# Kernel optimization log

Hardware: AMD Instinct MI355X
Metric: run time of the kernel (lower is better)

The kernel has to match this reference:

```python
import jax, jax.numpy as jnp
import numpy as np

N_NODES = 100000
N_EDGES = 1600000
K_IND = 16          # num_indicator_weight (distance bins)
K_MLP = 16          # num_mlp_weight
DIM_HIDDEN = 64     # dim_mlp_hidden
DIST_MAX = 1.0      # distance_max
K = K_IND + K_MLP   # node feature dim / Dense output dim


def setup_inputs() -> dict:
    key = jax.random.key(0)
    ks = jax.random.split(key, 10)
    nodes = jax.random.normal(ks[0], (N_NODES, K), dtype=jnp.float32)
    distance = jax.random.uniform(ks[1], (N_EDGES,), dtype=jnp.float32) * DIST_MAX
    receivers = jnp.sort(jax.random.randint(ks[2], (N_EDGES,), 0, N_NODES, dtype=jnp.int32))
    senders = jax.random.randint(ks[3], (N_EDGES,), 0, N_NODES, dtype=jnp.int32)
    edges_padding = jnp.ones((N_EDGES,), dtype=jnp.float32)
    # MLPWeights params (Dense(1->H), Dense(H->K_MLP))
    w1 = jax.random.normal(ks[4], (1, DIM_HIDDEN), dtype=jnp.float32) / np.sqrt(1.0)
    b1 = jnp.zeros((DIM_HIDDEN,), dtype=jnp.float32)
    w2 = jax.random.normal(ks[5], (DIM_HIDDEN, K_MLP), dtype=jnp.float32) / np.sqrt(DIM_HIDDEN)
    b2 = jnp.zeros((K_MLP,), dtype=jnp.float32)
    # PowerDifference params (a=0.5, b=2)
    a = jnp.array([0.5], dtype=jnp.float32)
    b = jnp.array([2.0], dtype=jnp.float32)
    # gamma_self (no bias), gamma_gathered (with bias), both Dense(K->K)
    wg_self = jax.random.normal(ks[6], (K, K), dtype=jnp.float32) / np.sqrt(K)
    wg_gath = jax.random.normal(ks[7], (K, K), dtype=jnp.float32) / np.sqrt(K)
    bg_gath = jnp.zeros((K,), dtype=jnp.float32)
    return {"nodes": nodes, "distance": distance, "edges_padding": edges_padding,
            "receivers": receivers, "senders": senders,
            "w1": w1, "b1": b1, "w2": w2, "b2": b2,
            "a": a, "b": b, "wg_self": wg_self, "wg_gath": wg_gath, "bg_gath": bg_gath}


def _normalize_edges(edges, seg_ids, num_segments):
    sums = jax.ops.segment_sum(edges, seg_ids, num_segments=num_segments, indices_are_sorted=True)
    return edges / (sums[seg_ids] + 1e-5)


def _softmax_edges(edges, seg_ids, num_segments):
    maxs = jax.ops.segment_max(edges, seg_ids, num_segments=num_segments, indices_are_sorted=True)
    e = jnp.exp(edges - maxs[seg_ids])
    sums = jax.ops.segment_sum(e, seg_ids, num_segments=num_segments, indices_are_sorted=True)
    return e / sums[seg_ids]


def reference(nodes, distance, edges_padding, receivers, senders,
              w1, b1, w2, b2, a, b, wg_self, wg_gath, bg_gath):
    n = nodes.shape[0]
    d = distance[:, None]                                   # [E,1]
    # IndicatorWeights: bin membership via heaviside of product
    bins = jnp.linspace(0.0, DIST_MAX, K_IND + 1, dtype=nodes.dtype)
    indicator = jnp.heaviside((bins[None, :-1] - d) * (d - bins[None, 1:]), 0.0)  # [E,K_IND]
    indicator_w = _normalize_edges(indicator, receivers, n)
    # MLPWeights: Dense -> relu -> Dense, then segment softmax
    mlp = jax.nn.relu(d @ w1 + b1) @ w2 + b2                # [E,K_MLP]
    mlp_w = _softmax_edges(mlp, receivers, n)
    weights = jnp.concatenate([indicator_w, mlp_w], axis=1) * edges_padding[:, None]  # [E,K]
    # PowerDifference on gathered node pairs
    a_c = jnp.clip(a, 0.0, 1.0)
    b_c = jnp.abs(b)
    edge_pds = jnp.power(jnp.abs(a_c * nodes[receivers] - (1.0 - a_c) * nodes[senders]), b_c)  # [E,K]
    gathered = jax.ops.segment_sum(weights * edge_pds, receivers, num_segments=n, indices_are_sorted=True)  # [N,K]
    out = jax.nn.relu(nodes @ wg_self + (gathered @ wg_gath + bg_gath))
    return out
```

## Files before the change

### kernel.cpp

```cpp
#include <hip/hip_runtime.h>
#include <math.h>

#define K_TOT 32
#define K_IND 16
#define K_MLP 16
#define DHID  64


__global__ void prep_kernel(const int* __restrict__ recv, int E, int N,
                            const float* __restrict__ w1,
                            const float* __restrict__ b1,
                            const float* __restrict__ w2,
                            float* __restrict__ wsP,
                            float* __restrict__ wsN,
                            int* __restrict__ wsflag,
                            int* __restrict__ rp) {
    if (blockIdx.x == 0 && threadIdx.x < 64) {
        int t = threadIdx.x;
        if (t < K_MLP) {
            float P = 0.f, Nn = 0.f;
            for (int j = 0; j < DHID; ++j) {
                float w = w1[j];
                float v = w2[j * K_MLP + t];
                P  += fmaxf(w, 0.f) * v;
                Nn += fminf(w, 0.f) * v;
            }
            wsP[t] = P; wsN[t] = Nn;
        }
        bool nz = (b1[t] != 0.f);
        unsigned long long mask = __ballot(nz);
        if (t == 0) *wsflag = (mask == 0ull) ? 1 : 0;
    }
    int tid = blockIdx.x * blockDim.x + threadIdx.x;
    if (tid <= N) {
        int lo = 0, hi = E;
        while (lo < hi) {
            int mid = (lo + hi) >> 1;
            if (recv[mid] < tid) lo = mid + 1; else hi = mid;
        }
        rp[tid] = lo;
    }
}

__global__ __launch_bounds__(256) void graph_kernel(
        const float* __restrict__ nodes,
        const float* __restrict__ dist,
        const float* __restrict__ padv,
        const int*   __restrict__ send,
        const float* __restrict__ w1,
        const float* __restrict__ b1,
        const float* __restrict__ w2,
        const float* __restrict__ b2,
        const float* __restrict__ a_p,
        const float* __restrict__ b_p,
        const float* __restrict__ wg_self,
        const float* __restrict__ wg_gath,
        const float* __restrict__ bg,
        const float* __restrict__ wsP,
        const float* __restrict__ wsN,
        const int*   __restrict__ wsflag,
        const int*   __restrict__ rp,
        float* __restrict__ out,
        int N) {
    int wave = blockIdx.x * (blockDim.x >> 6) + (threadIdx.x >> 6);
    if (wave >= N) return;
    int n    = wave;
    int lane = threadIdx.x & 63;
    int eg   = lane >> 4;
    int cc   = lane & 15;

    float a_c = fminf(fmaxf(a_p[0], 0.f), 1.f);
    float am  = 1.f - a_c;
    float bc  = fabsf(b_p[0]);
    bool  fastf = (*wsflag != 0) && (bc == 2.0f);

    float Pk = wsP[cc];
    float Nk = wsN[cc];

    const float* nrow = nodes + n * K_TOT;
    float nr0 = nrow[cc];
    float nr1 = nrow[cc + 16];
    float anr0 = a_c * nr0;
    float anr1 = a_c * nr1;

    int e0 = rp[n], eEnd = rp[n + 1];
    int len = eEnd - e0;

    float lo = (float)cc * 0.0625f;
    float hi = lo + 0.0625f;

    float cnt = 0.f, si = 0.f;
    float l = 0.f, acc = 0.f;
    float g_ind, g_mlp;

    int egb = eg << 2;

    if (__builtin_amdgcn_readfirstlane((int)fastf)) {
        float dm = 0.f;
        for (int base = 0; base < len; base += 64) {
            int idx = base + lane;
            int cmax = len - 1;
            idx = idx < cmax ? idx : cmax;
            dm = fmaxf(dm, fabsf(dist[e0 + idx]));
        }
#pragma unroll
        for (int off = 32; off; off >>= 1) dm = fmaxf(dm, __shfl_xor(dm, off));
        float negM = -fmaxf(fabsf(Pk), fabsf(Nk)) * dm;

        for (int base = 0; base < len; base += 64) {
            int rem = len - base;
            int ci = base + lane;
            int cmax = len - 1;
            ci = ci < cmax ? ci : cmax;
            int e = e0 + ci;
            float dl = dist[e];
            int   sl = send[e];
            float pl = padv[e];
            int nG = (rem + 3) >> 2;
            nG = nG < 16 ? nG : 16;
            int byteIdx = egb;
            for (int g2 = 0; g2 < nG; ++g2, byteIdx += 16) {
                float d  = __int_as_float(__builtin_amdgcn_ds_bpermute(byteIdx, __float_as_int(dl)));
                int   s  = __builtin_amdgcn_ds_bpermute(byteIdx, sl);
                float pe = __int_as_float(__builtin_amdgcn_ds_bpermute(byteIdx, __float_as_int(pl)));
                bool valid = (base + (g2 << 2) + eg) < len;

                const float* nsrow = nodes + (s * K_TOT + cc);
                float ns0 = nsrow[0];
                float ns1 = nsrow[16];

                float t0 = fmaf(-am, ns0, anr0);
                float t1 = fmaf(-am, ns1, anr1);
                float pd0 = t0 * t0;
                float pd1 = t1 * t1;

                bool inb = valid && (d > lo) && (d < hi);
                cnt += inb ? 1.f : 0.f;
                si  += inb ? pe * pd0 : 0.f;

                float q = (d > 0.f) ? Pk : Nk;
                float p = __expf(fmaf(d, q, negM));
                p = valid ? p : 0.f;
                l += p;
                acc = fmaf(p, pe * pd1, acc);
            }
        }

#pragma unroll
        for (int off = 16; off <= 32; off <<= 1) {
            cnt += __shfl_xor(cnt, off);
            si  += __shfl_xor(si,  off);
            l   += __shfl_xor(l,   off);
            acc += __shfl_xor(acc, off);
        }
        g_ind = si / (cnt + 1e-5f);
        g_mlp = (l > 0.f) ? (acc / l) : 0.f;
    } else {
        float m_on = -INFINITY;
        for (int i = eg; i < len; i += 4) {
            int e = e0 + i;
            float d  = dist[e];
            int   s  = send[e];
            float pe = padv[e];
            const float* nsrow = nodes + (s * K_TOT + cc);
            float ns0 = nsrow[0];
            float ns1 = nsrow[16];
            float t0 = fabsf(fmaf(-am, ns0, anr0));
            float t1 = fabsf(fmaf(-am, ns1, anr1));
            float pd0 = powf(t0, bc);
            float pd1 = powf(t1, bc);

            bool inb = (d > lo) && (d < hi);
            cnt += inb ? 1.f : 0.f;
            si  += inb ? pe * pd0 : 0.f;

            float mlp = 0.f;
            for (int j = 0; j < DHID; ++j) {
                float h = fmaxf(fmaf(d, w1[j], b1[j]), 0.f);
                mlp = fmaf(h, w2[j * K_MLP + cc], mlp);
            }
            float mn = fmaxf(m_on, mlp);
            float al = (m_on == -INFINITY) ? 0.f : __expf(m_on - mn);
            float p  = __expf(mlp - mn);
            l   = fmaf(l, al, p);
            acc = fmaf(acc, al, p * pe * pd1);
            m_on = mn;
        }
#pragma unroll
        for (int off = 16; off <= 32; off <<= 1) {
            cnt += __shfl_xor(cnt, off);
            si  += __shfl_xor(si,  off);
            float m2 = __shfl_xor(m_on, off), l2 = __shfl_xor(l, off), a2 = __shfl_xor(acc, off);
            float mn = fmaxf(m_on, m2);
            float f1 = (m_on == -INFINITY) ? 0.f : __expf(m_on - mn);
            float f2 = (m2   == -INFINITY) ? 0.f : __expf(m2 - mn);
            l   = l * f1 + l2 * f2;
            acc = acc * f1 + a2 * f2;
            m_on = mn;
        }
        g_ind = si / (cnt + 1e-5f);
        g_mlp = (l > 0.f) ? (acc / l) : 0.f;
    }

    int h  = lane >> 5;
    int oc = lane & 31;
    float pre_g = ((lane >> 4) & 1) ? g_mlp : g_ind;
    float pre_n = ((lane >> 4) & 1) ? nr1 : nr0;

    float o = 0.f;
    int jbase = h * 16;
#pragma unroll
    for (int jj = 0; jj < 16; ++jj) {
        int j = jbase + jj;
        float gj = __shfl(pre_g, j);
        float nj = __shfl(pre_n, j);
        o = fmaf(nj, wg_self[j * K_TOT + oc], o);
        o = fmaf(gj, wg_gath[j * K_TOT + oc], o);
    }
    o += __shfl_xor(o, 32);
    if (h == 0) {
        out[n * K_TOT + oc] = fmaxf(o + bg[oc], 0.f);
    }
}

extern "C" void kernel_launch(void* const* d_in, const int* in_sizes, int n_in,
                              void* d_out, int out_size, void* d_ws, size_t ws_size,
                              hipStream_t stream) {
    const float* nodes   = (const float*)d_in[0];
    const float* dist    = (const float*)d_in[1];
    const float* padv    = (const float*)d_in[2];
    const int*   recv    = (const int*)d_in[3];
    const int*   send    = (const int*)d_in[4];
    const float* w1      = (const float*)d_in[5];
    const float* b1      = (const float*)d_in[6];
    const float* w2      = (const float*)d_in[7];
    const float* b2      = (const float*)d_in[8];
    const float* a_p     = (const float*)d_in[9];
    const float* b_p     = (const float*)d_in[10];
    const float* wg_self = (const float*)d_in[11];
    const float* wg_gath = (const float*)d_in[12];
    const float* bg      = (const float*)d_in[13];
    float* out = (float*)d_out;

    int N = in_sizes[0] / K_TOT;
    int E = in_sizes[1];

    float* wsf    = (float*)d_ws;
    float* wsP    = wsf;
    float* wsN    = wsf + 16;
    int*   wsflag = (int*)d_ws + 32;
    int*   rp     = (int*)d_ws + 64;

    prep_kernel<<<(N + 1 + 255) / 256, 256, 0, stream>>>(recv, E, N, w1, b1, w2,
                                                         wsP, wsN, wsflag, rp);
    graph_kernel<<<(N + 3) / 4, 256, 0, stream>>>(
        nodes, dist, padv, send, w1, b1, w2, b2, a_p, b_p,
        wg_self, wg_gath, bg, wsP, wsN, wsflag, rp, out, N);
}
```

Baseline: 179.0 us.

## Process four nodes per wavefront, one 16-lane quarter per node

Measured after the change: 214.0 us. +19.6%, slower.

```diff
diff --git a/kernel.cpp b/kernel.cpp
--- a/kernel.cpp
+++ b/kernel.cpp
@@ -42,7 +42,7 @@
     }
 }
 
-__global__ __launch_bounds__(256) void graph_kernel(
+__global__ __launch_bounds__(256) void graph4_kernel(
         const float* __restrict__ nodes,
         const float* __restrict__ dist,
         const float* __restrict__ padv,
@@ -50,7 +50,6 @@
         const float* __restrict__ w1,
         const float* __restrict__ b1,
         const float* __restrict__ w2,
-        const float* __restrict__ b2,
         const float* __restrict__ a_p,
         const float* __restrict__ b_p,
         const float* __restrict__ wg_self,
@@ -62,29 +61,28 @@
         const int*   __restrict__ rp,
         float* __restrict__ out,
         int N) {
-    int wave = blockIdx.x * (blockDim.x >> 6) + (threadIdx.x >> 6);
-    if (wave >= N) return;
-    int n    = wave;
+    int wave  = blockIdx.x * 4 + (threadIdx.x >> 6);
+    int nbase = wave * 4;
+    if (nbase >= N) return;
     int lane = threadIdx.x & 63;
-    int eg   = lane >> 4;
+    int q    = lane >> 4;
     int cc   = lane & 15;
 
     float a_c = fminf(fmaxf(a_p[0], 0.f), 1.f);
     float am  = 1.f - a_c;
     float bc  = fabsf(b_p[0]);
-    bool  fastf = (*wsflag != 0) && (bc == 2.0f);
-
-    float Pk = wsP[cc];
-    float Nk = wsN[cc];
-
-    const float* nrow = nodes + n * K_TOT;
-    float nr0 = nrow[cc];
-    float nr1 = nrow[cc + 16];
-    float anr0 = a_c * nr0;
-    float anr1 = a_c * nr1;
-
-    int e0 = rp[n], eEnd = rp[n + 1];
-    int len = eEnd - e0;
+    float Pk  = wsP[cc];
+    float Nk  = wsN[cc];
+
+    int n  = nbase + q;
+    int nl = (n < N) ? n : N - 1;
+    int e0 = rp[nl], e1 = rp[nl + 1];
+    int len = (n < N) ? (e1 - e0) : 0;
+    int eb  = (len > 0) ? e0 : 0;
+
+    float nr0 = nodes[nl * K_TOT + cc];
+    float nr1 = nodes[nl * K_TOT + cc + 16];
+    float anr0 = a_c * nr0, anr1 = a_c * nr1;
 
     float lo = (float)cc * 0.0625f;
     float hi = lo + 0.0625f;
@@ -93,133 +91,128 @@
     float l = 0.f, acc = 0.f;
     float g_ind, g_mlp;
 
-    int egb = eg << 2;
+    bool fastf = (*wsflag != 0) && (bc == 2.0f);
 
     if (__builtin_amdgcn_readfirstlane((int)fastf)) {
         float dm = 0.f;
-        for (int base = 0; base < len; base += 64) {
-            int idx = base + lane;
-            int cmax = len - 1;
-            idx = idx < cmax ? idx : cmax;
-            dm = fmaxf(dm, fabsf(dist[e0 + idx]));
-        }
-#pragma unroll
-        for (int off = 32; off; off >>= 1) dm = fmaxf(dm, __shfl_xor(dm, off));
+        for (int i = cc; i < len; i += 16) dm = fmaxf(dm, fabsf(dist[e0 + i]));
+        dm = fmaxf(dm, __shfl_xor(dm, 1, 16));
+        dm = fmaxf(dm, __shfl_xor(dm, 2, 16));
+        dm = fmaxf(dm, __shfl_xor(dm, 4, 16));
+        dm = fmaxf(dm, __shfl_xor(dm, 8, 16));
         float negM = -fmaxf(fabsf(Pk), fabsf(Nk)) * dm;
 
-        for (int base = 0; base < len; base += 64) {
-            int rem = len - base;
-            int ci = base + lane;
-            int cmax = len - 1;
-            ci = ci < cmax ? ci : cmax;
-            int e = e0 + ci;
-            float dl = dist[e];
-            int   sl = send[e];
-            float pl = padv[e];
-            int nG = (rem + 3) >> 2;
-            nG = nG < 16 ? nG : 16;
-            int byteIdx = egb;
-            for (int g2 = 0; g2 < nG; ++g2, byteIdx += 16) {
-                float d  = __int_as_float(__builtin_amdgcn_ds_bpermute(byteIdx, __float_as_int(dl)));
-                int   s  = __builtin_amdgcn_ds_bpermute(byteIdx, sl);
-                float pe = __int_as_float(__builtin_amdgcn_ds_bpermute(byteIdx, __float_as_int(pl)));
-                bool valid = (base + (g2 << 2) + eg) < len;
-
-                const float* nsrow = nodes + (s * K_TOT + cc);
-                float ns0 = nsrow[0];
-                float ns1 = nsrow[16];
-
-                float t0 = fmaf(-am, ns0, anr0);
-                float t1 = fmaf(-am, ns1, anr1);
-                float pd0 = t0 * t0;
-                float pd1 = t1 * t1;
-
-                bool inb = valid && (d > lo) && (d < hi);
-                cnt += inb ? 1.f : 0.f;
-                si  += inb ? pe * pd0 : 0.f;
-
-                float q = (d > 0.f) ? Pk : Nk;
-                float p = __expf(fmaf(d, q, negM));
-                p = valid ? p : 0.f;
-                l += p;
-                acc = fmaf(p, pe * pd1, acc);
-            }
-        }
-
-#pragma unroll
-        for (int off = 16; off <= 32; off <<= 1) {
-            cnt += __shfl_xor(cnt, off);
-            si  += __shfl_xor(si,  off);
-            l   += __shfl_xor(l,   off);
-            acc += __shfl_xor(acc, off);
-        }
+        int T = len;
+        { int t2 = __shfl_xor(T, 16); T = T > t2 ? T : t2; }
+        { int t2 = __shfl_xor(T, 32); T = T > t2 ? T : t2; }
+        int last = (len > 0) ? (len - 1) : 0;
+
+#define IT_BODY(I)                                                        \
+        {                                                                 \
+            int  ii = (I) < last ? (I) : last;                            \
+            bool valid = (I) < len;                                       \
+            int  idx = eb + ii;                                           \
+            float d  = dist[idx];                                         \
+            int   s  = send[idx];                                         \
+            float pe = padv[idx];                                         \
+            const float* nsr = nodes + (s * K_TOT + cc);                  \
+            float ns0 = nsr[0], ns1 = nsr[16];                            \
+            float t0 = fmaf(-am, ns0, anr0);                              \
+            float t1 = fmaf(-am, ns1, anr1);                              \
+            float pd0 = t0 * t0, pd1 = t1 * t1;                           \
+            bool inb = valid && (d > lo) && (d < hi);                     \
+            cnt += inb ? 1.f : 0.f;                                       \
+            si   = inb ? fmaf(pe, pd0, si) : si;                          \
+            float qq = (d > 0.f) ? Pk : Nk;                               \
+            float p = __expf(fmaf(d, qq, negM));                          \
+            p = valid ? p : 0.f;                                          \
+            l += p;                                                       \
+            acc = fmaf(p, pe * pd1, acc);                                 \
+        }
+        int i = 0;
+        for (; i + 2 <= T; i += 2) { IT_BODY(i) IT_BODY(i + 1) }
+        if (i < T) { IT_BODY(i) }
+#undef IT_BODY
+
         g_ind = si / (cnt + 1e-5f);
         g_mlp = (l > 0.f) ? (acc / l) : 0.f;
     } else {
-        float m_on = -INFINITY;
-        for (int i = eg; i < len; i += 4) {
-            int e = e0 + i;
-            float d  = dist[e];
-            int   s  = send[e];
-            float pe = padv[e];
-            const float* nsrow = nodes + (s * K_TOT + cc);
-            float ns0 = nsrow[0];
-            float ns1 = nsrow[16];
-            float t0 = fabsf(fmaf(-am, ns0, anr0));
-            float t1 = fabsf(fmaf(-am, ns1, anr1));
-            float pd0 = powf(t0, bc);
-            float pd1 = powf(t1, bc);
-
-            bool inb = (d > lo) && (d < hi);
-            cnt += inb ? 1.f : 0.f;
-            si  += inb ? pe * pd0 : 0.f;
-
-            float mlp = 0.f;
-            for (int j = 0; j < DHID; ++j) {
-                float h = fmaxf(fmaf(d, w1[j], b1[j]), 0.f);
-                mlp = fmaf(h, w2[j * K_MLP + cc], mlp);
+        g_ind = 0.f; g_mlp = 0.f;
+        int eg = lane >> 4;
+        for (int t = 0; t < 4; ++t) {
+            int nn = nbase + t;
+            float gi = 0.f, gm = 0.f;
+            if (nn < N) {
+                const float* nrow = nodes + nn * K_TOT;
+                float xr0 = nrow[cc], xr1 = nrow[cc + 16];
+                float ax0 = a_c * xr0, ax1 = a_c * xr1;
+                int ee0 = rp[nn], ee1 = rp[nn + 1];
+                float tc = 0.f, ts = 0.f, tl = 0.f, ta = 0.f, m_on = -INFINITY;
+                for (int i2 = ee0 + eg; i2 < ee1; i2 += 4) {
+                    float d  = dist[i2];
+                    int   s  = send[i2];
+                    float pe = padv[i2];
+                    const float* nsr = nodes + (s * K_TOT + cc);
+                    float ns0 = nsr[0], ns1 = nsr[16];
+                    float t0 = fabsf(fmaf(-am, ns0, ax0));
+                    float t1 = fabsf(fmaf(-am, ns1, ax1));
+                    float pd0 = powf(t0, bc), pd1 = powf(t1, bc);
+                    bool inb = (d > lo) && (d < hi);
+                    tc += inb ? 1.f : 0.f;
+                    ts += inb ? pe * pd0 : 0.f;
+                    float mlp = 0.f;
+                    for (int j = 0; j < DHID; ++j) {
+                        float h = fmaxf(fmaf(d, w1[j], b1[j]), 0.f);
+                        mlp = fmaf(h, w2[j * K_MLP + cc], mlp);
+                    }
+                    float mn = fmaxf(m_on, mlp);
+                    float al = (m_on == -INFINITY) ? 0.f : __expf(m_on - mn);
+                    float pp = __expf(mlp - mn);
+                    tl = fmaf(tl, al, pp);
+                    ta = fmaf(ta, al, pp * pe * pd1);
+                    m_on = mn;
+                }
+#pragma unroll
+                for (int off = 16; off <= 32; off <<= 1) {
+                    tc += __shfl_xor(tc, off);
+                    ts += __shfl_xor(ts, off);
+                    float m2 = __shfl_xor(m_on, off), l2 = __shfl_xor(tl, off), a2 = __shfl_xor(ta, off);
+                    float mn = fmaxf(m_on, m2);
+                    float f1 = (m_on == -INFINITY) ? 0.f : __expf(m_on - mn);
+                    float f2 = (m2   == -INFINITY) ? 0.f : __expf(m2 - mn);
+                    tl = tl * f1 + l2 * f2;
+                    ta = ta * f1 + a2 * f2;
+                    m_on = mn;
+                }
+                gi = ts / (tc + 1e-5f);
+                gm = (tl > 0.f) ? (ta / tl) : 0.f;
             }
-            float mn = fmaxf(m_on, mlp);
-            float al = (m_on == -INFINITY) ? 0.f : __expf(m_on - mn);
-            float p  = __expf(mlp - mn);
-            l   = fmaf(l, al, p);
-            acc = fmaf(acc, al, p * pe * pd1);
-            m_on = mn;
-        }
+            if (q == t) { g_ind = gi; g_mlp = gm; }
+        }
+    }
+
+    int half = lane >> 5;
+    int oc   = lane & 31;
+    int jb   = half << 5;
 #pragma unroll
-        for (int off = 16; off <= 32; off <<= 1) {
-            cnt += __shfl_xor(cnt, off);
-            si  += __shfl_xor(si,  off);
-            float m2 = __shfl_xor(m_on, off), l2 = __shfl_xor(l, off), a2 = __shfl_xor(acc, off);
-            float mn = fmaxf(m_on, m2);
-            float f1 = (m_on == -INFINITY) ? 0.f : __expf(m_on - mn);
-            float f2 = (m2   == -INFINITY) ? 0.f : __expf(m2 - mn);
-            l   = l * f1 + l2 * f2;
-            acc = acc * f1 + a2 * f2;
-            m_on = mn;
-        }
-        g_ind = si / (cnt + 1e-5f);
-        g_mlp = (l > 0.f) ? (acc / l) : 0.f;
-    }
-
-    int h  = lane >> 5;
-    int oc = lane & 31;
-    float pre_g = ((lane >> 4) & 1) ? g_mlp : g_ind;
-    float pre_n = ((lane >> 4) & 1) ? nr1 : nr0;
-
-    float o = 0.f;
-    int jbase = h * 16;
+    for (int pass = 0; pass < 2; ++pass) {
+        int tnode = nbase + 2 * pass + half;
+        int src = (2 * pass + half) * 16 + (oc & 15);
+        float sgi = __shfl(g_ind, src);
+        float sgm = __shfl(g_mlp, src);
+        float sn0 = __shfl(nr0, src);
+        float sn1 = __shfl(nr1, src);
+        float pre_g = (oc < 16) ? sgi : sgm;
+        float pre_n = (oc < 16) ? sn0 : sn1;
+        float o = 0.f;
 #pragma unroll
-    for (int jj = 0; jj < 16; ++jj) {
-        int j = jbase + jj;
-        float gj = __shfl(pre_g, j);
-        float nj = __shfl(pre_n, j);
-        o = fmaf(nj, wg_self[j * K_TOT + oc], o);
-        o = fmaf(gj, wg_gath[j * K_TOT + oc], o);
-    }
-    o += __shfl_xor(o, 32);
-    if (h == 0) {
-        out[n * K_TOT + oc] = fmaxf(o + bg[oc], 0.f);
+        for (int j = 0; j < 32; ++j) {
+            float gj = __shfl(pre_g, jb + j);
+            float nj = __shfl(pre_n, jb + j);
+            o = fmaf(nj, wg_self[j * K_TOT + oc], o);
+            o = fmaf(gj, wg_gath[j * K_TOT + oc], o);
+        }
+        if (tnode < N) out[tnode * K_TOT + oc] = fmaxf(o + bg[oc], 0.f);
     }
 }
 
@@ -234,7 +227,6 @@
     const float* w1      = (const float*)d_in[5];
     const float* b1      = (const float*)d_in[6];
     const float* w2      = (const float*)d_in[7];
-    const float* b2      = (const float*)d_in[8];
     const float* a_p     = (const float*)d_in[9];
     const float* b_p     = (const float*)d_in[10];
     const float* wg_self = (const float*)d_in[11];
@@ -253,7 +245,8 @@
 
     prep_kernel<<<(N + 1 + 255) / 256, 256, 0, stream>>>(recv, E, N, w1, b1, w2,
                                                          wsP, wsN, wsflag, rp);
-    graph_kernel<<<(N + 3) / 4, 256, 0, stream>>>(
-        nodes, dist, padv, send, w1, b1, w2, b2, a_p, b_p,
+    int nwaves = (N + 3) / 4;
+    graph4_kernel<<<(nwaves + 3) / 4, 256, 0, stream>>>(
+        nodes, dist, padv, send, w1, b1, w2, a_p, b_p,
         wg_self, wg_gath, bg, wsP, wsN, wsflag, rp, out, N);
 }
```
